# Kernel tuning notes

Hardware: AMD Instinct MI355X
Metric: run time of the kernel (lower is better)

## Reference

```python
import jax, jax.numpy as jnp
import numpy as np


def _make_pairs(n):
    # full permutation of n items with diagonal removed, same as make_pair()
    i, j = np.meshgrid(np.arange(n), np.arange(n), indexing='ij')
    keep = (i != j).reshape(-1)
    return i.reshape(-1)[keep], j.reshape(-1)[keep]


def setup_inputs() -> dict:
    key = jax.random.key(0)
    k1, k2, k3 = jax.random.split(key, 3)
    B, N, D, C = 4, 512, 128, 101
    ci, cj = _make_pairs(N)                      # R = N*(N-1) proposal pairs
    conn_arr = jnp.stack([jnp.asarray(ci, jnp.int64), jnp.asarray(cj, jnp.int64)], axis=1)
    R = conn_arr.shape[0]
    rel_det_prob = jax.random.uniform(k1, (B, R, C), dtype=jnp.float32)
    det_scores = jax.random.uniform(k2, (B, D), dtype=jnp.float32)
    prop_idx = jax.random.randint(k3, (B, D), 0, N).astype(jnp.int64)
    return {
        'rel_det_prob': rel_det_prob,
        'det_scores': det_scores,
        'conn_arr': conn_arr,
        'prop_idx': prop_idx,
        'topk': 100,
    }


def reference(rel_det_prob, det_scores, conn_arr, prop_idx, topk):
    B, R, C = rel_det_prob.shape
    D = prop_idx.shape[1]
    # static detection pair index lists (make_pair over detections)
    pi_np, pj_np = _make_pairs(D)
    pi = jnp.asarray(pi_np)                      # [P]
    pj = jnp.asarray(pj_np)
    # sort connection pair keys once for O(log R) matching (replaces the
    # per-pair eq/nonzero scan in the original)
    M = jnp.max(conn_arr) + 1
    conn_key = conn_arr[:, 0] * M + conn_arr[:, 1]          # [R]
    order = jnp.argsort(conn_key)
    sorted_keys = conn_key[order]

    def per_image(rel_prob, p_idx, scores):
        # zero out background relation column, then per-pair class max
        rel_prob = rel_prob.at[:, 0].set(0.0)
        rel_cls = jnp.argmax(rel_prob, axis=1)              # [R]
        rel_cls_prob = jnp.max(rel_prob, axis=1)            # [R]
        # map detection pairs to proposal-index pairs
        a = p_idx[pi]
        b = p_idx[pj]
        valid = a != b                                      # non-dup filter
        key = a * M + b
        pos = jnp.clip(jnp.searchsorted(sorted_keys, key), 0, R - 1)
        matched = (sorted_keys[pos] == key) & valid
        midx = order[pos]                                   # row in conn_arr
        label = jnp.where(matched, rel_cls[midx], 0)
        prob = jnp.where(matched, rel_cls_prob[midx], 0.0)
        overall = prob * scores[pi] * scores[pj]
        # duplicate pairs were removed in the original; push them below any
        # real score so topk never selects them (probs are >= 0)
        overall = jnp.where(valid, overall, -1.0)
        top_vals, top_i = jax.lax.top_k(overall, topk)
        pairs = jnp.stack([pi[top_i], pj[top_i]], axis=1)   # [topk, 2]
        return pairs, label[top_i], prob[top_i], top_vals

    return jax.vmap(per_image)(rel_det_prob, prop_idx, det_scores)
```

## Files before the change

### kernel.cpp

```cpp
#include <hip/hip_runtime.h>

#define NPROP 512
#define BB 4
#define RR 261632
#define CC 101
#define DD 128
#define PP 16256
#define TOPK 100

__device__ __forceinline__ unsigned orderable(float f) {
    unsigned b = __float_as_uint(f);
    return (b & 0x80000000u) ? ~b : (b | 0x80000000u);
}
__device__ __forceinline__ float unorderable(unsigned u) {
    unsigned b = (u & 0x80000000u) ? (u & 0x7fffffffu) : ~u;
    return __uint_as_float(b);
}

__global__ void k_pairs(const float* __restrict__ rel, const float* __restrict__ scores,
                        const int* __restrict__ prop_idx,
                        float* __restrict__ overallA, float* __restrict__ probA,
                        int* __restrict__ labelA) {
    int g = blockIdx.x * (blockDim.x >> 6) + (threadIdx.x >> 6);
    int lane = threadIdx.x & 63;
    if (g >= BB * PP) return;
    int img = g / PP;
    int p = g - img * PP;
    int pi = p / 127;
    int jj = p - pi * 127;
    int pj = jj + (jj >= pi ? 1 : 0);
    int a = prop_idx[img * DD + pi];
    int b = prop_idx[img * DD + pj];
    if (a == b) {
        if (lane == 0) { overallA[g] = -1.0f; probA[g] = 0.0f; labelA[g] = 0; }
        return;
    }
    int midx = a * (NPROP - 1) + b - (b > a ? 1 : 0);
    const float* row = rel + ((size_t)img * RR + midx) * CC;
    float v = (lane == 0) ? 0.0f : row[lane];
    int idx = lane;
    int c2 = lane + 64;
    if (c2 < CC) {
        float v2 = row[c2];
        if (v2 > v) { v = v2; idx = c2; }
    }
#pragma unroll
    for (int m = 32; m >= 1; m >>= 1) {
        float ov = __shfl_xor(v, m);
        int   oi = __shfl_xor(idx, m);
        if (ov > v || (ov == v && oi < idx)) { v = ov; idx = oi; }
    }
    if (lane == 0) {
        float si = scores[img * DD + pi], sj = scores[img * DD + pj];
        probA[g] = v;
        labelA[g] = idx;
        overallA[g] = (v * si) * sj;
    }
}

__global__ __launch_bounds__(1024) void k_topk(const float* __restrict__ overallA,
                                               const float* __restrict__ probA,
                                               const int* __restrict__ labelA,
                                               float* __restrict__ out) {
    int img = blockIdx.x;
    int tid = threadIdx.x;
    int lane = tid & 63;
    __shared__ int cntS[32];
    __shared__ int sCnt;
    __shared__ unsigned long long cand[128];

    unsigned uv[16];
    const float* base = overallA + img * PP;
#pragma unroll
    for (int k = 0; k < 16; ++k) {
        int idx = tid + (k << 10);
        float f = (idx < PP) ? base[idx] : -3.0f;
        uv[k] = orderable(f);
    }
    if (tid < 32) cntS[tid] = 0;
    if (tid == 0) sCnt = 0;
    __syncthreads();

    unsigned P = 0;
    for (int bit = 31; bit >= 0; --bit) {
        unsigned trial = P | (1u << bit);
        int c = 0;
#pragma unroll
        for (int k = 0; k < 16; ++k) c += (uv[k] >= trial) ? 1 : 0;
#pragma unroll
        for (int m = 32; m >= 1; m >>= 1) c += __shfl_xor(c, m);
        if (lane == 0) atomicAdd(&cntS[bit], c);
        __syncthreads();
        if (cntS[bit] >= TOPK) P = trial;
    }

#pragma unroll
    for (int k = 0; k < 16; ++k) {
        if (uv[k] >= P) {
            int pos = atomicAdd(&sCnt, 1);
            if (pos < 128) {
                int idx = tid + (k << 10);
                cand[pos] = ((unsigned long long)uv[k] << 14) | (unsigned)(16383 - idx);
            }
        }
    }
    __syncthreads();
    int cnt = sCnt; if (cnt > 128) cnt = 128;
    if (tid < 128 && tid >= cnt) cand[tid] = 0ull;

    for (int kk = 2; kk <= 128; kk <<= 1) {
        for (int j = kk >> 1; j > 0; j >>= 1) {
            __syncthreads();
            if (tid < 128) {
                int ixj = tid ^ j;
                if (ixj > tid) {
                    unsigned long long a = cand[tid], b = cand[ixj];
                    bool desc = ((tid & kk) == 0);
                    bool sw = desc ? (a < b) : (a > b);
                    if (sw) { cand[tid] = b; cand[ixj] = a; }
                }
            }
        }
    }
    __syncthreads();

    if (tid < TOPK) {
        unsigned long long key = cand[tid];
        int idx = 16383 - (int)(key & 0x3FFFull);
        float val = unorderable((unsigned)(key >> 14));
        int pi = idx / 127;
        int jj = idx - pi * 127;
        int pj = jj + (jj >= pi ? 1 : 0);
        out[img * 2 * TOPK + 2 * tid]     = (float)pi;
        out[img * 2 * TOPK + 2 * tid + 1] = (float)pj;
        out[BB * 2 * TOPK + img * TOPK + tid] = (float)labelA[img * PP + idx];
        out[BB * 3 * TOPK + img * TOPK + tid] = probA[img * PP + idx];
        out[BB * 4 * TOPK + img * TOPK + tid] = val;
    }
}

extern "C" void kernel_launch(void* const* d_in, const int* in_sizes, int n_in,
                              void* d_out, int out_size, void* d_ws, size_t ws_size,
                              hipStream_t stream) {
    const float* rel      = (const float*)d_in[0];
    const float* scores   = (const float*)d_in[1];
    const int*   prop_idx = (const int*)d_in[3];
    float* out = (float*)d_out;

    char* ws = (char*)d_ws;
    float* overallA = (float*)(ws);
    float* probA    = (float*)(ws + 260096);
    int*   labelA   = (int*)(ws + 2 * 260096);

    k_pairs<<<(BB * PP) / 4, 256, 0, stream>>>(rel, scores, prop_idx,
                                               overallA, probA, labelA);
    k_topk<<<BB, 1024, 0, stream>>>(overallA, probA, labelA, out);
}
```

Baseline: 498.5 us.

## Use 2-bit radix steps, wave-aggregated candidate compaction, and rank-based topk sort

The top-k threshold search now resolves two bits per round by counting three trial thresholds at once. This halves the number of block-wide barriers and shared atomics rounds. Candidate compaction uses a wave ballot with a single atomic per wave instead of one atomic per element. The bitonic sort over 128 candidates, with its many barriers, is replaced by each thread counting how many keys beat its own and writing to that rank, at the cost of more comparisons per thread.

```diff
diff --git a/kernel.cpp b/kernel.cpp
--- a/kernel.cpp
+++ b/kernel.cpp
@@ -65,7 +65,7 @@
     int img = blockIdx.x;
     int tid = threadIdx.x;
     int lane = tid & 63;
-    __shared__ int cntS[32];
+    __shared__ int cntS[48];
     __shared__ int sCnt;
     __shared__ unsigned long long cand[128];
 
@@ -77,65 +77,80 @@
         float f = (idx < PP) ? base[idx] : -3.0f;
         uv[k] = orderable(f);
     }
-    if (tid < 32) cntS[tid] = 0;
+    if (tid < 48) cntS[tid] = 0;
     if (tid == 0) sCnt = 0;
     __syncthreads();
 
     unsigned P = 0;
-    for (int bit = 31; bit >= 0; --bit) {
-        unsigned trial = P | (1u << bit);
-        int c = 0;
+    for (int r = 0; r < 16; ++r) {
+        int shift = 30 - 2 * r;
+        unsigned t1 = P | (1u << shift);
+        unsigned t2 = P | (2u << shift);
+        unsigned t3 = P | (3u << shift);
+        int c1 = 0, c2 = 0, c3 = 0;
 #pragma unroll
-        for (int k = 0; k < 16; ++k) c += (uv[k] >= trial) ? 1 : 0;
+        for (int k = 0; k < 16; ++k) {
+            unsigned u = uv[k];
+            c1 += (u >= t1) ? 1 : 0;
+            c2 += (u >= t2) ? 1 : 0;
+            c3 += (u >= t3) ? 1 : 0;
+        }
 #pragma unroll
-        for (int m = 32; m >= 1; m >>= 1) c += __shfl_xor(c, m);
-        if (lane == 0) atomicAdd(&cntS[bit], c);
+        for (int m = 32; m >= 1; m >>= 1) {
+            c1 += __shfl_xor(c1, m);
+            c2 += __shfl_xor(c2, m);
+            c3 += __shfl_xor(c3, m);
+        }
+        if (lane == 0) {
+            atomicAdd(&cntS[r * 3 + 0], c1);
+            atomicAdd(&cntS[r * 3 + 1], c2);
+            atomicAdd(&cntS[r * 3 + 2], c3);
+        }
         __syncthreads();
-        if (cntS[bit] >= TOPK) P = trial;
+        if      (cntS[r * 3 + 2] >= TOPK) P = t3;
+        else if (cntS[r * 3 + 1] >= TOPK) P = t2;
+        else if (cntS[r * 3 + 0] >= TOPK) P = t1;
     }
 
 #pragma unroll
     for (int k = 0; k < 16; ++k) {
-        if (uv[k] >= P) {
-            int pos = atomicAdd(&sCnt, 1);
-            if (pos < 128) {
-                int idx = tid + (k << 10);
-                cand[pos] = ((unsigned long long)uv[k] << 14) | (unsigned)(16383 - idx);
+        bool pred = (uv[k] >= P);
+        unsigned long long mask = __ballot(pred);
+        if (mask) {
+            int wbase = 0;
+            if (lane == 0) wbase = atomicAdd(&sCnt, __popcll(mask));
+            wbase = __shfl(wbase, 0);
+            if (pred) {
+                int pos = wbase + (int)__popcll(mask & ((1ull << lane) - 1ull));
+                if (pos < 128) {
+                    int idx = tid + (k << 10);
+                    cand[pos] = ((unsigned long long)uv[k] << 14) | (unsigned)(16383 - idx);
+                }
             }
         }
     }
     __syncthreads();
     int cnt = sCnt; if (cnt > 128) cnt = 128;
     if (tid < 128 && tid >= cnt) cand[tid] = 0ull;
-
-    for (int kk = 2; kk <= 128; kk <<= 1) {
-        for (int j = kk >> 1; j > 0; j >>= 1) {
-            __syncthreads();
-            if (tid < 128) {
-                int ixj = tid ^ j;
-                if (ixj > tid) {
-                    unsigned long long a = cand[tid], b = cand[ixj];
-                    bool desc = ((tid & kk) == 0);
-                    bool sw = desc ? (a < b) : (a > b);
-                    if (sw) { cand[tid] = b; cand[ixj] = a; }
-                }
-            }
-        }
-    }
     __syncthreads();
 
-    if (tid < TOPK) {
-        unsigned long long key = cand[tid];
-        int idx = 16383 - (int)(key & 0x3FFFull);
-        float val = unorderable((unsigned)(key >> 14));
-        int pi = idx / 127;
-        int jj = idx - pi * 127;
-        int pj = jj + (jj >= pi ? 1 : 0);
-        out[img * 2 * TOPK + 2 * tid]     = (float)pi;
-        out[img * 2 * TOPK + 2 * tid + 1] = (float)pj;
-        out[BB * 2 * TOPK + img * TOPK + tid] = (float)labelA[img * PP + idx];
-        out[BB * 3 * TOPK + img * TOPK + tid] = probA[img * PP + idx];
-        out[BB * 4 * TOPK + img * TOPK + tid] = val;
+    if (tid < 128) {
+        unsigned long long mine = cand[tid];
+        int rank = 0;
+        for (int j = 0; j < 128; ++j)
+            rank += (cand[j] > mine) ? 1 : 0;
+        if (tid < cnt && rank < TOPK) {
+            int idx = 16383 - (int)(mine & 0x3FFFull);
+            float val = unorderable((unsigned)(mine >> 14));
+            int pi = idx / 127;
+            int jj = idx - pi * 127;
+            int pj = jj + (jj >= pi ? 1 : 0);
+            out[img * 2 * TOPK + 2 * rank]     = (float)pi;
+            out[img * 2 * TOPK + 2 * rank + 1] = (float)pj;
+            out[BB * 2 * TOPK + img * TOPK + rank] = (float)labelA[img * PP + idx];
+            out[BB * 3 * TOPK + img * TOPK + rank] = probA[img * PP + idx];
+            out[BB * 4 * TOPK + img * TOPK + rank] = val;
+        }
     }
 }
 
```

After: 501.7 us. About the same (+0.6%).
